# Kernel tuning notes

Hardware: AMD Instinct MI355X
Metric: run time of the kernel (lower is better)

Reference implementation:

```python
import jax, jax.numpy as jnp
import numpy as np

N = 100000      # num nodes (in_features)
E = 1600000     # num edges
P = 100000      # num pos/neg label edges
EMB = 64        # embedding dim (hardcoded 64 in Encoder)
HID = 128       # 2 * out_channels
OUT = 64        # out_channels
EPS = 1e-15     # PyG GAE EPS
MAX_LOGSTD = 10.0


def setup_inputs() -> dict:
    key = jax.random.key(0)
    ks = jax.random.split(key, 10)
    emb_weight = jax.random.normal(ks[0], (N, EMB), dtype=jnp.float32) * 0.1
    edge_index = jax.random.randint(ks[1], (2, E), 0, N, dtype=jnp.int64)
    pos_edge_label_index = jax.random.randint(ks[2], (2, P), 0, N, dtype=jnp.int64)
    neg_edge_label_index = jax.random.randint(ks[3], (2, P), 0, N, dtype=jnp.int64)
    W1 = jax.random.normal(ks[4], (EMB, HID), dtype=jnp.float32) / np.sqrt(EMB)
    b1 = jnp.zeros((HID,), dtype=jnp.float32)
    W_mu = jax.random.normal(ks[5], (HID, OUT), dtype=jnp.float32) / np.sqrt(HID)
    b_mu = jnp.zeros((OUT,), dtype=jnp.float32)
    W_ls = jax.random.normal(ks[6], (HID, OUT), dtype=jnp.float32) / np.sqrt(HID)
    b_ls = jnp.zeros((OUT,), dtype=jnp.float32)
    return {
        'emb_weight': emb_weight, 'edge_index': edge_index,
        'W1': W1, 'b1': b1, 'W_mu': W_mu, 'b_mu': b_mu, 'W_ls': W_ls, 'b_ls': b_ls,
        'pos_edge_label_index': pos_edge_label_index,
        'neg_edge_label_index': neg_edge_label_index,
    }


def gcn_conv(x, src, dst, deg_inv_sqrt, W, b):
    # GCNConv with added self-loops and symmetric normalization:
    # out = D^{-1/2} (A + I) D^{-1/2} (x W) + b
    h = x @ W                                  # [N, F_out]
    norm = deg_inv_sqrt[src] * deg_inv_sqrt[dst]          # [E]
    agg = jax.ops.segment_sum(h[src] * norm[:, None], dst, num_segments=N)
    agg = agg + h * (deg_inv_sqrt * deg_inv_sqrt)[:, None]  # self-loop term
    return agg + b


def reference(emb_weight, edge_index, W1, b1, W_mu, b_mu, W_ls, b_ls,
              pos_edge_label_index, neg_edge_label_index):
    src, dst = edge_index[0], edge_index[1]
    # degree includes self-loop weight 1
    deg = jax.ops.segment_sum(jnp.ones((E,), dtype=emb_weight.dtype), dst, num_segments=N) + 1.0
    deg_inv_sqrt = jax.lax.rsqrt(deg)

    h = jax.nn.relu(gcn_conv(emb_weight, src, dst, deg_inv_sqrt, W1, b1))
    mu = gcn_conv(h, src, dst, deg_inv_sqrt, W_mu, b_mu)
    logstd = jnp.minimum(gcn_conv(h, src, dst, deg_inv_sqrt, W_ls, b_ls), MAX_LOGSTD)
    z = mu  # eval-mode reparametrize returns mu

    # recon_loss: inner-product decoder + BCE on pos/neg label edges
    ps, pd = pos_edge_label_index[0], pos_edge_label_index[1]
    ns, nd = neg_edge_label_index[0], neg_edge_label_index[1]
    pos_p = jax.nn.sigmoid(jnp.sum(z[ps] * z[pd], axis=-1))
    neg_p = jax.nn.sigmoid(jnp.sum(z[ns] * z[nd], axis=-1))
    pos_loss = -jnp.mean(jnp.log(pos_p + EPS))
    neg_loss = -jnp.mean(jnp.log(1.0 - neg_p + EPS))
    loss = pos_loss + neg_loss
    return z, logstd, loss
```

## Files before the change

### kernel.cpp

```cpp
#include <hip/hip_runtime.h>
#include <hip/hip_bf16.h>
#include <hip/hip_fp16.h>

#define NN 100000
#define NE 1600000
#define NP 100000

typedef _Float16 h2v __attribute__((ext_vector_type(2)));

__device__ __forceinline__ float fdot2u(uint a, uint b, float c) {
    union { uint u; h2v h; } ua, ub;
    ua.u = a; ub.u = b;
    return __builtin_amdgcn_fdot2(ua.h, ub.h, c, false);
}

__device__ __forceinline__ uint packh2(float lo, float hi) {
    __half2 h = __floats2half2_rn(lo, hi);
    return *(uint*)&h;
}

__device__ __forceinline__ void h8_to_f(const uint4 u, float* f) {
    const __half2* hp = (const __half2*)&u;
    float2 t0 = __half22float2(hp[0]), t1 = __half22float2(hp[1]);
    float2 t2 = __half22float2(hp[2]), t3 = __half22float2(hp[3]);
    f[0] = t0.x; f[1] = t0.y; f[2] = t1.x; f[3] = t1.y;
    f[4] = t2.x; f[5] = t2.y; f[6] = t3.x; f[7] = t3.y;
}

__device__ __forceinline__ void add8(const uint4 u, float* acc) {
    float f[8]; h8_to_f(u, f);
#pragma unroll
    for (int i = 0; i < 8; ++i) acc[i] += f[i];
}

#define RNG 400
#define NBK 250
#define K_A 8000
#define CAPB 12288

__global__ __launch_bounds__(256) void k_hist(const int* __restrict__ ei,
                                              int* __restrict__ bcnt) {
    __shared__ int hist[NBK];
    int tid = threadIdx.x;
    int e0 = blockIdx.x * K_A;
    for (int i = tid; i < NBK; i += 256) hist[i] = 0;
    __syncthreads();
    for (int i = tid; i < K_A; i += 256) atomicAdd(&hist[ei[NE + e0 + i] / RNG], 1);
    __syncthreads();
    for (int i = tid; i < NBK; i += 256) if (hist[i]) atomicAdd(&bcnt[i], hist[i]);
}

__global__ __launch_bounds__(256) void k_bscan(const int* __restrict__ bcnt,
                                               int* __restrict__ bbase,
                                               int* __restrict__ gcnt) {
    __shared__ int c[NBK];
    int tid = threadIdx.x;
    if (tid < NBK) c[tid] = bcnt[tid];
    __syncthreads();
    if (tid < 64) {
        int run = 0;
        for (int g = 0; g < NBK; g += 64) {
            int idx = g + tid;
            int v = (idx < NBK) ? c[idx] : 0;
            int inc = v;
#pragma unroll
            for (int off = 1; off < 64; off <<= 1) {
                int t2 = __shfl_up(inc, off);
                if (tid >= off) inc += t2;
            }
            if (idx < NBK) { int ex = run + inc - v; bbase[idx] = ex; gcnt[idx] = ex; }
            run += __shfl(inc, 63);
        }
        if (tid == 0) bbase[NBK] = run;
    }
}

__global__ __launch_bounds__(256) void k_binA(const int* __restrict__ ei,
                                              int* __restrict__ gcnt,
                                              int* __restrict__ edges) {
    __shared__ int buf[K_A];
    __shared__ int hist[NBK], lofs[NBK + 1], lcnt[NBK], gbase[NBK];
    int tid = threadIdx.x;
    int e0 = blockIdx.x * K_A;
    for (int i = tid; i < NBK; i += 256) { hist[i] = 0; lcnt[i] = 0; }
    __syncthreads();
    for (int i = tid; i < K_A; i += 256) atomicAdd(&hist[ei[NE + e0 + i] / RNG], 1);
    __syncthreads();
    if (tid < 64) {
        int run = 0;
        for (int g = 0; g < NBK; g += 64) {
            int idx = g + tid;
            int v = (idx < NBK) ? hist[idx] : 0;
            int inc = v;
#pragma unroll
            for (int off = 1; off < 64; off <<= 1) {
                int t2 = __shfl_up(inc, off);
                if (tid >= off) inc += t2;
            }
            if (idx < NBK) lofs[idx] = run + inc - v;
            run += __shfl(inc, 63);
        }
        if (tid == 0) lofs[NBK] = run;
    }
    for (int i = tid; i < NBK; i += 256) gbase[i] = atomicAdd(&gcnt[i], hist[i]);
    __syncthreads();
    for (int i = tid; i < K_A; i += 256) {
        int s = ei[e0 + i], d = ei[NE + e0 + i];
        int b = d / RNG;
        int dl = d - b * RNG;
        int p = lofs[b] + atomicAdd(&lcnt[b], 1);
        buf[p] = s | (dl << 17);
    }
    __syncthreads();
    for (int j = tid; j < K_A; j += 256) {
        int loB = 0, hiB = NBK;
        while (hiB - loB > 1) {
            int mid = (loB + hiB) >> 1;
            if (lofs[mid] <= j) loB = mid; else hiB = mid;
        }
        edges[gbase[loB] + (j - lofs[loB])] = buf[j];
    }
}

__global__ __launch_bounds__(256) void k_binB(const int* __restrict__ bbase,
                                              int* __restrict__ edges,
                                              int* __restrict__ rowptr,
                                              float* __restrict__ dinv) {
    __shared__ int buf[CAPB];
    __shared__ int hist[RNG], lrp[RNG], lcnt[RNG];
    int tid = threadIdx.x;
    int b = blockIdx.x;
    int lo = b * RNG;
    int base = bbase[b], n = bbase[b + 1] - base;
    for (int i = tid; i < RNG; i += 256) { hist[i] = 0; lcnt[i] = 0; }
    __syncthreads();
    for (int i = tid; i < n; i += 256)
        atomicAdd(&hist[((unsigned)edges[base + i]) >> 17], 1);
    __syncthreads();
    if (tid < 64) {
        int run = 0;
        for (int g = 0; g < RNG; g += 64) {
            int idx = g + tid;
            int v = (idx < RNG) ? hist[idx] : 0;
            int inc = v;
#pragma unroll
            for (int off = 1; off < 64; off <<= 1) {
                int t2 = __shfl_up(inc, off);
                if (tid >= off) inc += t2;
            }
            if (idx < RNG) lrp[idx] = run + inc - v;
            run += __shfl(inc, 63);
        }
    }
    __syncthreads();
    for (int i = tid; i < RNG; i += 256) {
        dinv[lo + i] = rsqrtf((float)hist[i] + 1.0f);
        rowptr[lo + i] = base + lrp[i];
    }
    if (b == NBK - 1 && tid == 0) rowptr[NN] = base + n;
    int ovS0 = -1, ovS1 = -1, ovR0 = 0, ovR1 = 0;
    for (int i = tid; i < n; i += 256) {
        int rec = edges[base + i];
        int dl = ((unsigned)rec) >> 17;
        int src = rec & 0x1FFFF;
        int slot = lrp[dl] + atomicAdd(&lcnt[dl], 1);
        if (slot < CAPB) buf[slot] = src;
        else if (ovS0 < 0) { ovS0 = slot; ovR0 = src; }
        else { ovS1 = slot; ovR1 = src; }
    }
    __syncthreads();
    int lim = n < CAPB ? n : CAPB;
    for (int i = tid; i < lim; i += 256) edges[base + i] = buf[i];
    if (ovS0 >= 0) edges[base + ovS0] = ovR0;
    if (ovS1 >= 0) edges[base + ovS1] = ovR1;
}

__global__ void k_cvt(const float4* __restrict__ in4, const float* __restrict__ dinv,
                      uint4* __restrict__ out) {
    int t = blockIdx.x * blockDim.x + threadIdx.x;
    if (t >= NN * 8) return;
    float dv = dinv[t >> 3];
    float4 a = in4[t * 2], b = in4[t * 2 + 1];
    union { __half2 h[4]; uint4 u; } pk;
    pk.h[0] = __floats2half2_rn(a.x * dv, a.y * dv);
    pk.h[1] = __floats2half2_rn(a.z * dv, a.w * dv);
    pk.h[2] = __floats2half2_rn(b.x * dv, b.y * dv);
    pk.h[3] = __floats2half2_rn(b.z * dv, b.w * dv);
    out[t] = pk.u;
}

__global__ __launch_bounds__(512) void k_l1(const uint4* __restrict__ x16,
                                            const float* __restrict__ dinv,
                                            const int* __restrict__ rowptr,
                                            const int* __restrict__ edges,
                                            const float4* __restrict__ W1_4,
                                            const float* __restrict__ b1,
                                            uint2* __restrict__ h16) {
    __shared__ uint4 w16h[32 * 32];
    __shared__ uint rows16[64 * 32];
    int t = threadIdx.x;
    int base = blockIdx.x * 64;
#pragma unroll
    for (int i = 0; i < 2; ++i) {
        int idx = t + i * 512;
        int kp = idx >> 5, jg = idx & 31;
        float4 we = W1_4[(2 * kp) * 32 + jg];
        float4 wo = W1_4[(2 * kp + 1) * 32 + jg];
        w16h[idx] = make_uint4(packh2(we.x, wo.x), packh2(we.y, wo.y),
                               packh2(we.z, wo.z), packh2(we.w, wo.w));
    }
    __syncthreads();
    int w = t >> 6;
    {
        int rl = (t >> 3) & 7, q = t & 7;
        int lrow = w * 8 + rl;
        int r = base + lrow;
        if (r < NN) {
            float acc[8];
            h8_to_f(x16[(size_t)r * 8 + q], acc);
            int j = rowptr[r], j1 = rowptr[r + 1];
            for (; j + 8 <= j1; j += 8) {
                int e[8]; uint4 v[8];
#pragma unroll
                for (int i = 0; i < 8; ++i) e[i] = edges[j + i];
#pragma unroll
                for (int i = 0; i < 8; ++i) v[i] = x16[(size_t)e[i] * 8 + q];
#pragma unroll
                for (int i = 0; i < 8; ++i) add8(v[i], acc);
            }
            if (j + 4 <= j1) {
                int e[4]; uint4 v[4];
#pragma unroll
                for (int i = 0; i < 4; ++i) e[i] = edges[j + i];
#pragma unroll
                for (int i = 0; i < 4; ++i) v[i] = x16[(size_t)e[i] * 8 + q];
#pragma unroll
                for (int i = 0; i < 4; ++i) add8(v[i], acc);
                j += 4;
            }
            for (; j < j1; ++j) add8(x16[(size_t)edges[j] * 8 + q], acc);
            float dr = dinv[r];
#pragma unroll
            for (int i = 0; i < 8; ++i) acc[i] *= dr;
#pragma unroll
            for (int i = 0; i < 4; ++i)
                rows16[lrow * 32 + 4 * q + i] = packh2(acc[2 * i], acc[2 * i + 1]);
        }
    }
    __builtin_amdgcn_wave_barrier();
    int lane = t & 63;
    int jg = lane & 31, rsel = lane >> 5;
    int r0 = w * 8 + rsel * 4;
    float4 bias = ((const float4*)b1)[jg];
    float acc[4][4];
#pragma unroll
    for (int r2 = 0; r2 < 4; ++r2) {
        acc[r2][0] = bias.x; acc[r2][1] = bias.y; acc[r2][2] = bias.z; acc[r2][3] = bias.w;
    }
#pragma unroll 4
    for (int kp = 0; kp < 32; ++kp) {
        uint f0 = rows16[(r0 + 0) * 32 + kp];
        uint f1 = rows16[(r0 + 1) * 32 + kp];
        uint f2 = rows16[(r0 + 2) * 32 + kp];
        uint f3 = rows16[(r0 + 3) * 32 + kp];
        uint4 wv = w16h[kp * 32 + jg];
        acc[0][0] = fdot2u(f0, wv.x, acc[0][0]); acc[0][1] = fdot2u(f0, wv.y, acc[0][1]);
        acc[0][2] = fdot2u(f0, wv.z, acc[0][2]); acc[0][3] = fdot2u(f0, wv.w, acc[0][3]);
        acc[1][0] = fdot2u(f1, wv.x, acc[1][0]); acc[1][1] = fdot2u(f1, wv.y, acc[1][1]);
        acc[1][2] = fdot2u(f1, wv.z, acc[1][2]); acc[1][3] = fdot2u(f1, wv.w, acc[1][3]);
        acc[2][0] = fdot2u(f2, wv.x, acc[2][0]); acc[2][1] = fdot2u(f2, wv.y, acc[2][1]);
        acc[2][2] = fdot2u(f2, wv.z, acc[2][2]); acc[2][3] = fdot2u(f2, wv.w, acc[2][3]);
        acc[3][0] = fdot2u(f3, wv.x, acc[3][0]); acc[3][1] = fdot2u(f3, wv.y, acc[3][1]);
        acc[3][2] = fdot2u(f3, wv.z, acc[3][2]); acc[3][3] = fdot2u(f3, wv.w, acc[3][3]);
    }
#pragma unroll
    for (int r2 = 0; r2 < 4; ++r2) {
        int row = base + r0 + r2;
        if (row < NN) {
            float dv = dinv[row];
            union { __half2 h[2]; uint2 u; } pk;
            pk.h[0] = __floats2half2_rn(fmaxf(acc[r2][0], 0.0f) * dv,
                                        fmaxf(acc[r2][1], 0.0f) * dv);
            pk.h[1] = __floats2half2_rn(fmaxf(acc[r2][2], 0.0f) * dv,
                                        fmaxf(acc[r2][3], 0.0f) * dv);
            h16[(size_t)row * 32 + jg] = pk.u;
        }
    }
}

__global__ __launch_bounds__(512) void k_l2(const uint4* __restrict__ x16,
                                            const float* __restrict__ dinv,
                                            const int* __restrict__ rowptr,
                                            const int* __restrict__ edges,
                                            const float4* __restrict__ Wmu4,
                                            const float* __restrict__ bmu,
                                            const float4* __restrict__ Wls4,
                                            const float* __restrict__ bls,
                                            float* __restrict__ out,
                                            uint2* __restrict__ z16) {
    __shared__ uint4 w16h[64 * 32];
    __shared__ uint rows16[32 * 64];
    int t = threadIdx.x;
    int base = blockIdx.x * 32;
#pragma unroll
    for (int i = 0; i < 4; ++i) {
        int idx = t + i * 512;
        int kp = idx >> 5, jg = idx & 31;
        int jj = (jg < 16) ? jg : (jg - 16);
        const float4* W = (jg < 16) ? Wmu4 : Wls4;
        float4 we = W[(2 * kp) * 16 + jj];
        float4 wo = W[(2 * kp + 1) * 16 + jj];
        w16h[idx] = make_uint4(packh2(we.x, wo.x), packh2(we.y, wo.y),
                               packh2(we.z, wo.z), packh2(we.w, wo.w));
    }
    __syncthreads();
    int w = t >> 6;
    {
        int rl = (t >> 4) & 3, q = t & 15;
        int lrow = w * 4 + rl;
        int r = base + lrow;
        float acc[8];
        h8_to_f(x16[(size_t)r * 16 + q], acc);
        int j = rowptr[r], j1 = rowptr[r + 1];
        for (; j + 8 <= j1; j += 8) {
            int e[8]; uint4 v[8];
#pragma unroll
            for (int i = 0; i < 8; ++i) e[i] = edges[j + i];
#pragma unroll
            for (int i = 0; i < 8; ++i) v[i] = x16[(size_t)e[i] * 16 + q];
#pragma unroll
            for (int i = 0; i < 8; ++i) add8(v[i], acc);
        }
        if (j + 4 <= j1) {
            int e[4]; uint4 v[4];
#pragma unroll
            for (int i = 0; i < 4; ++i) e[i] = edges[j + i];
#pragma unroll
            for (int i = 0; i < 4; ++i) v[i] = x16[(size_t)e[i] * 16 + q];
#pragma unroll
            for (int i = 0; i < 4; ++i) add8(v[i], acc);
            j += 4;
        }
        for (; j < j1; ++j) add8(x16[(size_t)edges[j] * 16 + q], acc);
        float dr = dinv[r];
#pragma unroll
        for (int i = 0; i < 8; ++i) acc[i] *= dr;
#pragma unroll
        for (int i = 0; i < 4; ++i)
            rows16[lrow * 64 + 4 * q + i] = packh2(acc[2 * i], acc[2 * i + 1]);
    }
    __builtin_amdgcn_wave_barrier();
    int lane = t & 63;
    int jg = lane & 31, rsel = lane >> 5;
    int r0 = w * 4 + rsel * 2;
    float4 bias = (jg < 16) ? ((const float4*)bmu)[jg] : ((const float4*)bls)[jg - 16];
    float acc[2][4];
#pragma unroll
    for (int r2 = 0; r2 < 2; ++r2) {
        acc[r2][0] = bias.x; acc[r2][1] = bias.y; acc[r2][2] = bias.z; acc[r2][3] = bias.w;
    }
#pragma unroll 8
    for (int kp = 0; kp < 64; ++kp) {
        uint f0 = rows16[(r0 + 0) * 64 + kp];
        uint f1 = rows16[(r0 + 1) * 64 + kp];
        uint4 wv = w16h[kp * 32 + jg];
        acc[0][0] = fdot2u(f0, wv.x, acc[0][0]); acc[0][1] = fdot2u(f0, wv.y, acc[0][1]);
        acc[0][2] = fdot2u(f0, wv.z, acc[0][2]); acc[0][3] = fdot2u(f0, wv.w, acc[0][3]);
        acc[1][0] = fdot2u(f1, wv.x, acc[1][0]); acc[1][1] = fdot2u(f1, wv.y, acc[1][1]);
        acc[1][2] = fdot2u(f1, wv.z, acc[1][2]); acc[1][3] = fdot2u(f1, wv.w, acc[1][3]);
    }
    float4* out4 = (float4*)out;
    if (jg < 16) {
#pragma unroll
        for (int r2 = 0; r2 < 2; ++r2) {
            int row = base + r0 + r2;
            out4[(size_t)row * 16 + jg] =
                make_float4(acc[r2][0], acc[r2][1], acc[r2][2], acc[r2][3]);
            union { __half2 h[2]; uint2 u; } pk;
            pk.h[0] = __floats2half2_rn(acc[r2][0], acc[r2][1]);
            pk.h[1] = __floats2half2_rn(acc[r2][2], acc[r2][3]);
            z16[(size_t)row * 16 + jg] = pk.u;
        }
    } else {
#pragma unroll
        for (int r2 = 0; r2 < 2; ++r2) {
            int row = base + r0 + r2;
            float4 o = make_float4(fminf(acc[r2][0], 10.0f), fminf(acc[r2][1], 10.0f),
                                   fminf(acc[r2][2], 10.0f), fminf(acc[r2][3], 10.0f));
            out4[(size_t)NN * 16 + (size_t)row * 16 + (jg - 16)] = o;
        }
    }
}

__global__ __launch_bounds__(256) void k_loss(const int* __restrict__ pos,
                                              const int* __restrict__ neg,
                                              const uint2* __restrict__ z16,
                                              float* __restrict__ accum) {
    int t = blockIdx.x * blockDim.x + threadIdx.x;
    int grp = t >> 4, q = t & 15;
    int e0 = grp * 4;
    bool isNeg = e0 >= NP;
    const int* idx = isNeg ? neg : pos;
    int eb = isNeg ? e0 - NP : e0;
    int a0 = idx[eb + 0], b0 = idx[NP + eb + 0];
    int a1 = idx[eb + 1], b1 = idx[NP + eb + 1];
    int a2 = idx[eb + 2], b2 = idx[NP + eb + 2];
    int a3 = idx[eb + 3], b3 = idx[NP + eb + 3];
    uint2 ua0 = z16[(size_t)a0 * 16 + q], ub0 = z16[(size_t)b0 * 16 + q];
    uint2 ua1 = z16[(size_t)a1 * 16 + q], ub1 = z16[(size_t)b1 * 16 + q];
    uint2 ua2 = z16[(size_t)a2 * 16 + q], ub2 = z16[(size_t)b2 * 16 + q];
    uint2 ua3 = z16[(size_t)a3 * 16 + q], ub3 = z16[(size_t)b3 * 16 + q];
    float d0 = fdot2u(ua0.y, ub0.y, fdot2u(ua0.x, ub0.x, 0.0f));
    float d1 = fdot2u(ua1.y, ub1.y, fdot2u(ua1.x, ub1.x, 0.0f));
    float d2 = fdot2u(ua2.y, ub2.y, fdot2u(ua2.x, ub2.x, 0.0f));
    float d3 = fdot2u(ua3.y, ub3.y, fdot2u(ua3.x, ub3.x, 0.0f));
#pragma unroll
    for (int off = 1; off < 16; off <<= 1) {
        d0 += __shfl_xor(d0, off);
        d1 += __shfl_xor(d1, off);
        d2 += __shfl_xor(d2, off);
        d3 += __shfl_xor(d3, off);
    }
    __shared__ float bsum[2];
    if (threadIdx.x < 2) bsum[threadIdx.x] = 0.0f;
    __syncthreads();
    if (q == 0) {
        float term;
        if (isNeg) {
            term = logf(1.0f - 1.0f / (1.0f + expf(-d0)) + 1e-15f)
                 + logf(1.0f - 1.0f / (1.0f + expf(-d1)) + 1e-15f)
                 + logf(1.0f - 1.0f / (1.0f + expf(-d2)) + 1e-15f)
                 + logf(1.0f - 1.0f / (1.0f + expf(-d3)) + 1e-15f);
        } else {
            term = logf(1.0f / (1.0f + expf(-d0)) + 1e-15f)
                 + logf(1.0f / (1.0f + expf(-d1)) + 1e-15f)
                 + logf(1.0f / (1.0f + expf(-d2)) + 1e-15f)
                 + logf(1.0f / (1.0f + expf(-d3)) + 1e-15f);
        }
        atomicAdd(&bsum[isNeg ? 1 : 0], term);
    }
    __syncthreads();
    if (threadIdx.x < 2) atomicAdd(&accum[threadIdx.x], bsum[threadIdx.x]);
}

__global__ void k_fin(const float* __restrict__ accum, float* __restrict__ out) {
    out[(size_t)NN * 128] = -(accum[0] + accum[1]) * (1.0f / (float)NP);
}

extern "C" void kernel_launch(void* const* d_in, const int* in_sizes, int n_in,
                              void* d_out, int out_size, void* d_ws, size_t ws_size,
                              hipStream_t stream) {
    const float* emb = (const float*)d_in[0];
    const int*   ei  = (const int*)d_in[1];
    const float* W1  = (const float*)d_in[2];
    const float* b1  = (const float*)d_in[3];
    const float* Wmu = (const float*)d_in[4];
    const float* bmu = (const float*)d_in[5];
    const float* Wls = (const float*)d_in[6];
    const float* bls = (const float*)d_in[7];
    const int*   pos = (const int*)d_in[8];
    const int*   neg = (const int*)d_in[9];
    float* out = (float*)d_out;

    char* ws = (char*)d_ws;
    float* dinv   = (float*)(ws);
    int*   rowptr = (int*)  (ws + (512 << 10));
    int*   bcnt   = (int*)  (ws + (1024 << 10));
    int*   bbase  = (int*)  (ws + (1028 << 10));
    int*   gcnt   = (int*)  (ws + (1032 << 10));
    float* accum  = (float*)(ws + (1040 << 10));
    const size_t OFF_EDGES = (2048 << 10);
    const size_t OFF_H16   = OFF_EDGES + (size_t)NE * 4;
    const size_t OFF_E16   = OFF_H16 + (size_t)NN * 128 * 2;
    int*   edges  = (int*)(ws + OFF_EDGES);
    uint2* h16    = (uint2*)(ws + OFF_H16);
    uint4* emb16  = (uint4*)(ws + OFF_E16);
    uint2* z16    = (uint2*)(ws + OFF_E16);

    hipMemsetAsync(bcnt, 0, NBK * sizeof(int), stream);
    hipMemsetAsync(accum, 0, 2 * sizeof(float), stream);

    k_hist <<<NE / K_A, 256, 0, stream>>>(ei, bcnt);
    k_bscan<<<1, 256, 0, stream>>>(bcnt, bbase, gcnt);
    k_binA <<<NE / K_A, 256, 0, stream>>>(ei, gcnt, edges);
    k_binB <<<NBK, 256, 0, stream>>>(bbase, edges, rowptr, dinv);

    k_cvt  <<<(NN * 8 + 255) / 256, 256, 0, stream>>>((const float4*)emb, dinv, emb16);

    k_l1<<<(NN + 63) / 64, 512, 0, stream>>>(emb16, dinv, rowptr, edges,
                                             (const float4*)W1, b1, h16);
    k_l2<<<NN / 32, 512, 0, stream>>>((const uint4*)h16, dinv, rowptr, edges,
                                      (const float4*)Wmu, bmu, (const float4*)Wls, bls,
                                      out, z16);

    k_loss<<<(2 * NP * 16) / (256 * 4), 256, 0, stream>>>(pos, neg, z16, accum);
    k_fin<<<1, 1, 0, stream>>>(accum, out);
}
```

Baseline: 279.3 us.

## Store per-block histograms, drop binning atomics, fuse loss finalize, widen loss loads

The histogram pass now writes per-block bucket counts instead of atomically accumulating global totals. The scan kernel computes each block's global base offsets directly, so the binning kernel no longer recounts its slice or does atomic base reservation. The loss kernel reads 16-byte fp16 chunks with 8 lanes per edge and finalizes the scalar with a last-block ticket, which removes the separate finalize launch and one memset. In exchange the single-block scan does serial loops over 200 block histograms, and the binning order becomes deterministic.

New measurement: 288.8 us. 1.03x slower.

```diff
diff --git a/kernel.cpp b/kernel.cpp
--- a/kernel.cpp
+++ b/kernel.cpp
@@ -33,13 +33,20 @@
     for (int i = 0; i < 8; ++i) acc[i] += f[i];
 }
 
+__device__ __forceinline__ float dot8h(uint4 a, uint4 b, float c) {
+    c = fdot2u(a.x, b.x, c); c = fdot2u(a.y, b.y, c);
+    c = fdot2u(a.z, b.z, c); c = fdot2u(a.w, b.w, c);
+    return c;
+}
+
 #define RNG 400
 #define NBK 250
 #define K_A 8000
+#define NBLKA (NE / K_A)
 #define CAPB 12288
 
 __global__ __launch_bounds__(256) void k_hist(const int* __restrict__ ei,
-                                              int* __restrict__ bcnt) {
+                                              int* __restrict__ hists) {
     __shared__ int hist[NBK];
     int tid = threadIdx.x;
     int e0 = blockIdx.x * K_A;
@@ -47,44 +54,61 @@
     __syncthreads();
     for (int i = tid; i < K_A; i += 256) atomicAdd(&hist[ei[NE + e0 + i] / RNG], 1);
     __syncthreads();
-    for (int i = tid; i < NBK; i += 256) if (hist[i]) atomicAdd(&bcnt[i], hist[i]);
-}
-
-__global__ __launch_bounds__(256) void k_bscan(const int* __restrict__ bcnt,
+    for (int i = tid; i < NBK; i += 256) hists[blockIdx.x * NBK + i] = hist[i];
+}
+
+__global__ __launch_bounds__(256) void k_bscan(const int* __restrict__ hists,
                                                int* __restrict__ bbase,
-                                               int* __restrict__ gcnt) {
-    __shared__ int c[NBK];
+                                               int* __restrict__ gbaseAll) {
+    __shared__ int tot[NBK];
+    __shared__ int bb[NBK + 1];
     int tid = threadIdx.x;
-    if (tid < NBK) c[tid] = bcnt[tid];
+    if (tid < NBK) {
+        int s = 0;
+        for (int blk = 0; blk < NBLKA; ++blk) s += hists[blk * NBK + tid];
+        tot[tid] = s;
+    }
     __syncthreads();
     if (tid < 64) {
         int run = 0;
         for (int g = 0; g < NBK; g += 64) {
             int idx = g + tid;
-            int v = (idx < NBK) ? c[idx] : 0;
+            int v = (idx < NBK) ? tot[idx] : 0;
             int inc = v;
 #pragma unroll
             for (int off = 1; off < 64; off <<= 1) {
                 int t2 = __shfl_up(inc, off);
                 if (tid >= off) inc += t2;
             }
-            if (idx < NBK) { int ex = run + inc - v; bbase[idx] = ex; gcnt[idx] = ex; }
+            if (idx < NBK) bb[idx] = run + inc - v;
             run += __shfl(inc, 63);
         }
-        if (tid == 0) bbase[NBK] = run;
+        if (tid == 0) bb[NBK] = run;
+    }
+    __syncthreads();
+    if (tid <= NBK) bbase[tid] = bb[tid];
+    if (tid < NBK) {
+        int run = bb[tid];
+        for (int blk = 0; blk < NBLKA; ++blk) {
+            gbaseAll[blk * NBK + tid] = run;
+            run += hists[blk * NBK + tid];
+        }
     }
 }
 
 __global__ __launch_bounds__(256) void k_binA(const int* __restrict__ ei,
-                                              int* __restrict__ gcnt,
+                                              const int* __restrict__ hists,
+                                              const int* __restrict__ gbaseAll,
                                               int* __restrict__ edges) {
     __shared__ int buf[K_A];
     __shared__ int hist[NBK], lofs[NBK + 1], lcnt[NBK], gbase[NBK];
-    int tid = threadIdx.x;
-    int e0 = blockIdx.x * K_A;
-    for (int i = tid; i < NBK; i += 256) { hist[i] = 0; lcnt[i] = 0; }
-    __syncthreads();
-    for (int i = tid; i < K_A; i += 256) atomicAdd(&hist[ei[NE + e0 + i] / RNG], 1);
+    int tid = threadIdx.x, blk = blockIdx.x;
+    int e0 = blk * K_A;
+    for (int i = tid; i < NBK; i += 256) {
+        hist[i]  = hists[blk * NBK + i];
+        gbase[i] = gbaseAll[blk * NBK + i];
+        lcnt[i]  = 0;
+    }
     __syncthreads();
     if (tid < 64) {
         int run = 0;
@@ -102,7 +126,6 @@
         }
         if (tid == 0) lofs[NBK] = run;
     }
-    for (int i = tid; i < NBK; i += 256) gbase[i] = atomicAdd(&gcnt[i], hist[i]);
     __syncthreads();
     for (int i = tid; i < K_A; i += 256) {
         int s = ei[e0 + i], d = ei[NE + e0 + i];
@@ -394,28 +417,30 @@
 
 __global__ __launch_bounds__(256) void k_loss(const int* __restrict__ pos,
                                               const int* __restrict__ neg,
-                                              const uint2* __restrict__ z16,
-                                              float* __restrict__ accum) {
+                                              const uint4* __restrict__ z4,
+                                              float* __restrict__ accum,
+                                              float* __restrict__ out) {
     int t = blockIdx.x * blockDim.x + threadIdx.x;
-    int grp = t >> 4, q = t & 15;
+    int grp = t >> 3, q = t & 7;
     int e0 = grp * 4;
+    bool valid = e0 < 2 * NP;
     bool isNeg = e0 >= NP;
     const int* idx = isNeg ? neg : pos;
-    int eb = isNeg ? e0 - NP : e0;
+    int eb = (valid && isNeg) ? e0 - NP : (valid ? e0 : 0);
     int a0 = idx[eb + 0], b0 = idx[NP + eb + 0];
     int a1 = idx[eb + 1], b1 = idx[NP + eb + 1];
     int a2 = idx[eb + 2], b2 = idx[NP + eb + 2];
     int a3 = idx[eb + 3], b3 = idx[NP + eb + 3];
-    uint2 ua0 = z16[(size_t)a0 * 16 + q], ub0 = z16[(size_t)b0 * 16 + q];
-    uint2 ua1 = z16[(size_t)a1 * 16 + q], ub1 = z16[(size_t)b1 * 16 + q];
-    uint2 ua2 = z16[(size_t)a2 * 16 + q], ub2 = z16[(size_t)b2 * 16 + q];
-    uint2 ua3 = z16[(size_t)a3 * 16 + q], ub3 = z16[(size_t)b3 * 16 + q];
-    float d0 = fdot2u(ua0.y, ub0.y, fdot2u(ua0.x, ub0.x, 0.0f));
-    float d1 = fdot2u(ua1.y, ub1.y, fdot2u(ua1.x, ub1.x, 0.0f));
-    float d2 = fdot2u(ua2.y, ub2.y, fdot2u(ua2.x, ub2.x, 0.0f));
-    float d3 = fdot2u(ua3.y, ub3.y, fdot2u(ua3.x, ub3.x, 0.0f));
-#pragma unroll
-    for (int off = 1; off < 16; off <<= 1) {
+    uint4 ua0 = z4[(size_t)a0 * 8 + q], ub0 = z4[(size_t)b0 * 8 + q];
+    uint4 ua1 = z4[(size_t)a1 * 8 + q], ub1 = z4[(size_t)b1 * 8 + q];
+    uint4 ua2 = z4[(size_t)a2 * 8 + q], ub2 = z4[(size_t)b2 * 8 + q];
+    uint4 ua3 = z4[(size_t)a3 * 8 + q], ub3 = z4[(size_t)b3 * 8 + q];
+    float d0 = dot8h(ua0, ub0, 0.0f);
+    float d1 = dot8h(ua1, ub1, 0.0f);
+    float d2 = dot8h(ua2, ub2, 0.0f);
+    float d3 = dot8h(ua3, ub3, 0.0f);
+#pragma unroll
+    for (int off = 1; off < 8; off <<= 1) {
         d0 += __shfl_xor(d0, off);
         d1 += __shfl_xor(d1, off);
         d2 += __shfl_xor(d2, off);
@@ -424,7 +449,7 @@
     __shared__ float bsum[2];
     if (threadIdx.x < 2) bsum[threadIdx.x] = 0.0f;
     __syncthreads();
-    if (q == 0) {
+    if (q == 0 && valid) {
         float term;
         if (isNeg) {
             term = logf(1.0f - 1.0f / (1.0f + expf(-d0)) + 1e-15f)
@@ -441,10 +466,13 @@
     }
     __syncthreads();
     if (threadIdx.x < 2) atomicAdd(&accum[threadIdx.x], bsum[threadIdx.x]);
-}
-
-__global__ void k_fin(const float* __restrict__ accum, float* __restrict__ out) {
-    out[(size_t)NN * 128] = -(accum[0] + accum[1]) * (1.0f / (float)NP);
+    if (threadIdx.x == 0) {
+        __threadfence();
+        int ticket = atomicAdd((int*)accum + 2, 1);
+        if (ticket == (int)gridDim.x - 1) {
+            out[(size_t)NN * 128] = -(accum[0] + accum[1]) * (1.0f / (float)NP);
+        }
+    }
 }
 
 extern "C" void kernel_launch(void* const* d_in, const int* in_sizes, int n_in,
@@ -463,12 +491,12 @@
     float* out = (float*)d_out;
 
     char* ws = (char*)d_ws;
-    float* dinv   = (float*)(ws);
-    int*   rowptr = (int*)  (ws + (512 << 10));
-    int*   bcnt   = (int*)  (ws + (1024 << 10));
-    int*   bbase  = (int*)  (ws + (1028 << 10));
-    int*   gcnt   = (int*)  (ws + (1032 << 10));
-    float* accum  = (float*)(ws + (1040 << 10));
+    float* dinv    = (float*)(ws);
+    int*   rowptr  = (int*)  (ws + (512 << 10));
+    int*   hists   = (int*)  (ws + (1024 << 10));
+    int*   gbaseAll= (int*)  (ws + (1280 << 10));
+    int*   bbase   = (int*)  (ws + (1536 << 10));
+    float* accum   = (float*)(ws + (1540 << 10));
     const size_t OFF_EDGES = (2048 << 10);
     const size_t OFF_H16   = OFF_EDGES + (size_t)NE * 4;
     const size_t OFF_E16   = OFF_H16 + (size_t)NN * 128 * 2;
@@ -477,12 +505,11 @@
     uint4* emb16  = (uint4*)(ws + OFF_E16);
     uint2* z16    = (uint2*)(ws + OFF_E16);
 
-    hipMemsetAsync(bcnt, 0, NBK * sizeof(int), stream);
-    hipMemsetAsync(accum, 0, 2 * sizeof(float), stream);
-
-    k_hist <<<NE / K_A, 256, 0, stream>>>(ei, bcnt);
-    k_bscan<<<1, 256, 0, stream>>>(bcnt, bbase, gcnt);
-    k_binA <<<NE / K_A, 256, 0, stream>>>(ei, gcnt, edges);
+    hipMemsetAsync(accum, 0, 16, stream);
+
+    k_hist <<<NBLKA, 256, 0, stream>>>(ei, hists);
+    k_bscan<<<1, 256, 0, stream>>>(hists, bbase, gbaseAll);
+    k_binA <<<NBLKA, 256, 0, stream>>>(ei, hists, gbaseAll, edges);
     k_binB <<<NBK, 256, 0, stream>>>(bbase, edges, rowptr, dinv);
 
     k_cvt  <<<(NN * 8 + 255) / 256, 256, 0, stream>>>((const float4*)emb, dinv, emb16);
@@ -493,6 +520,6 @@
                                       (const float4*)Wmu, bmu, (const float4*)Wls, bls,
                                       out, z16);
 
-    k_loss<<<(2 * NP * 16) / (256 * 4), 256, 0, stream>>>(pos, neg, z16, accum);
-    k_fin<<<1, 1, 0, stream>>>(accum, out);
-}
+    k_loss<<<(2 * NP + 127) / 128, 256, 0, stream>>>(pos, neg, (const uint4*)z16,
+                                                     accum, out);
+}
```
